# Kernel tuning notes

Hardware: AMD Instinct MI355X
Metric: run time of the kernel (lower is better)

## Reference

```python
import jax, jax.numpy as jnp
import numpy as np

B, S, D = 4, 8192, 512


def log_g(x):
    # torch: where(x>=0, log(relu(x)+0.5), -softplus(-x)); relu(x)+0.5 >= 0.5 so log is safe
    return jnp.where(x >= 0, jnp.log(jax.nn.relu(x) + 0.5), -jax.nn.softplus(-x))


def parallel_scan_log(log_coeffs, log_values):
    # log_coeffs: (B,S,D); log_values: (B,S+1,D)
    a_star = jnp.pad(jnp.cumsum(log_coeffs, axis=1), ((0, 0), (1, 0), (0, 0)))  # (B,S+1,D)
    log_h = a_star + jax.lax.cumlogsumexp(log_values - a_star, axis=1)
    return jnp.exp(log_h)[:, 1:]  # (B,S,D)


def setup_inputs() -> dict:
    key = jax.random.key(0)
    ks = jax.random.split(key, 7)
    scale = 1.0 / np.sqrt(D)
    x = jax.random.normal(ks[0], (B, S, D), dtype=jnp.float32)
    pre_h = jnp.zeros((B, 1, D), dtype=jnp.float32)
    Wf = jax.random.normal(ks[1], (D, D), dtype=jnp.float32) * scale
    bf = jax.random.normal(ks[2], (D,), dtype=jnp.float32) * 0.01
    Wi = jax.random.normal(ks[3], (D, D), dtype=jnp.float32) * scale
    bi = jax.random.normal(ks[4], (D,), dtype=jnp.float32) * 0.01
    Wh = jax.random.normal(ks[5], (D, D), dtype=jnp.float32) * scale
    bh = jax.random.normal(ks[6], (D,), dtype=jnp.float32) * 0.01
    return {"x": x, "pre_h": pre_h, "Wf": Wf, "bf": bf, "Wi": Wi, "bi": bi, "Wh": Wh, "bh": bh}


def reference(x, pre_h, Wf, bf, Wi, bi, Wh, bh):
    # gates: log(sigmoid(k)) = -softplus(-k)
    log_f = -jax.nn.softplus(-(jnp.einsum('bsd,de->bse', x, Wf) + bf))
    log_i = -jax.nn.softplus(-(jnp.einsum('bsd,de->bse', x, Wi) + bi))
    log_tilde_h = log_g(jnp.einsum('bsd,de->bse', x, Wh) + bh)
    log_pre_h = log_g(pre_h)  # (B,1,D)
    log_values = jnp.concatenate([log_pre_h, log_i + log_tilde_h], axis=1)  # (B,S+1,D)
    return parallel_scan_log(log_f, log_values)
```

## Files before the change

kernel.cpp:

```cpp
#include <hip/hip_runtime.h>
#include <hip/hip_bf16.h>

#define BATCH 4
#define SEQ   8192
#define DIM   512
#define M_TOT (BATCH*SEQ)
#define NCHUNK 128
#define CLEN   64

typedef __attribute__((ext_vector_type(4))) int int4v;
typedef __attribute__((ext_vector_type(8))) unsigned short ushort8v;

__device__ __forceinline__ float sigmoidf_(float x) {
    return 1.0f / (1.0f + __expf(-x));
}
__device__ __forceinline__ float gfun_(float x) {
    return (x >= 0.0f) ? (x + 0.5f) : sigmoidf_(x);
}

__device__ __forceinline__ void stage16(const void* g, void* lds) {
    __builtin_amdgcn_global_load_lds((const __attribute__((address_space(1))) void*)g,
                                     (__attribute__((address_space(3))) void*)lds,
                                     16, 0, 0);
}

__global__ __launch_bounds__(256) void quant_x(const float* __restrict__ x,
                                               char* __restrict__ xh, char* __restrict__ xl)
{
    const int t = blockIdx.x * 256 + threadIdx.x;
    float4 v = ((const float4*)x)[t];
    float vals[4] = {v.x, v.y, v.z, v.w};
    char hs[4], ls[4];
    #pragma unroll
    for (int e = 0; e < 4; ++e) {
        float c = fminf(fmaxf(vals[e], -15.8f), 15.8f);
        int q = (int)rintf(c * 2048.0f);
        int hi = (q + 128) >> 8;
        int lo = q - (hi << 8);
        hs[e] = (char)hi; ls[e] = (char)lo;
    }
    char4 hv = {hs[0], hs[1], hs[2], hs[3]};
    char4 lv = {ls[0], ls[1], ls[2], ls[3]};
    *(char4*)&xh[(size_t)t * 4] = hv;
    *(char4*)&xl[(size_t)t * 4] = lv;
}

__global__ __launch_bounds__(256) void quant_wT(
    const float* __restrict__ Wf, const float* __restrict__ Wi, const float* __restrict__ Wh,
    char* __restrict__ wth, char* __restrict__ wtl)
{
    __shared__ float tile[64][65];
    const int g = blockIdx.z;
    const float* W = (g == 0) ? Wf : (g == 1) ? Wi : Wh;
    const int k0 = blockIdx.x * 64, n0 = blockIdx.y * 64;
    const int c = threadIdx.x & 63, r4 = threadIdx.x >> 6;
    #pragma unroll
    for (int p = 0; p < 16; ++p) {
        int r = p * 4 + r4;
        tile[r][c] = W[(size_t)(k0 + r) * DIM + n0 + c];
    }
    __syncthreads();
    const size_t gbase = (size_t)g * DIM * DIM;
    #pragma unroll
    for (int p = 0; p < 16; ++p) {
        int nr = p * 4 + r4;
        float w = tile[c][nr];
        float cl = fminf(fmaxf(w, -0.49f), 0.49f);
        int q = (int)rintf(cl * 65536.0f);
        int hi = (q + 128) >> 8;
        int lo = q - (hi << 8);
        size_t o = gbase + (size_t)(n0 + nr) * DIM + k0 + c;
        wth[o] = (char)hi;
        wtl[o] = (char)lo;
    }
}

__global__ __launch_bounds__(512, 4) void gemm_i8(
    const char* __restrict__ xh, const char* __restrict__ xl,
    const char* __restrict__ wth, const char* __restrict__ wtl,
    const float* __restrict__ bfv, const float* __restrict__ biv, const float* __restrict__ bhv,
    float* __restrict__ fb, unsigned short* __restrict__ sib, unsigned short* __restrict__ ghb)
{
    __shared__ char smem[65536];
    char (*sA)[2][128][64] = (char (*)[2][128][64])smem;
    char (*sB)[2][128][64] = (char (*)[2][128][64])(smem + 32768);
    unsigned short (*lds16)[136] = (unsigned short (*)[136])smem;

    const int bid = blockIdx.x;
    const int xr  = bid & 7;
    const int t   = bid >> 3;
    const int mmt = t / 12;
    const int gn  = t - mmt * 12;
    const int g   = gn >> 2;
    const int n0  = (gn & 3) * 128;
    const int m0  = (xr + (mmt << 3)) * 128;

    const int tid  = threadIdx.x;
    const int wave = tid >> 6;
    const int lane = tid & 63;
    const int wi = wave >> 2, wj = wave & 3;

    const char* wh_g = wth + (size_t)g * DIM * DIM;
    const char* wl_g = wtl + (size_t)g * DIM * DIM;

    const int smm  = tid >> 2;
    const int skb  = (tid & 3) * 16;
    const int sksw = skb ^ (((smm >> 1) & 3) << 4);
    const int swrow = (tid >> 6) * 16;
    const char* gx_h = xh   + (size_t)(m0 + smm) * DIM + sksw;
    const char* gx_l = xl   + (size_t)(m0 + smm) * DIM + sksw;
    const char* gw_h = wh_g + (size_t)(n0 + smm) * DIM + sksw;
    const char* gw_l = wl_g + (size_t)(n0 + smm) * DIM + sksw;

    int4v P2[4][2], P1[4][2];
    const int4v zero = {0, 0, 0, 0};
    #pragma unroll
    for (int i = 0; i < 4; ++i)
        #pragma unroll
        for (int j = 0; j < 2; ++j) { P2[i][j] = zero; P1[i][j] = zero; }

    stage16(gx_h, &sA[0][0][swrow][0]);
    stage16(gx_l, &sA[0][1][swrow][0]);
    stage16(gw_h, &sB[0][0][swrow][0]);
    stage16(gw_l, &sB[0][1][swrow][0]);

    #pragma unroll
    for (int kt = 0; kt < 8; ++kt) {
        const int cur = kt & 1;
        if (kt < 7) {
            const int nb = cur ^ 1;
            const int ko = (kt + 1) * 64;
            stage16(gx_h + ko, &sA[nb][0][swrow][0]);
            stage16(gx_l + ko, &sA[nb][1][swrow][0]);
            stage16(gw_h + ko, &sB[nb][0][swrow][0]);
            stage16(gw_l + ko, &sB[nb][1][swrow][0]);
            asm volatile("s_waitcnt vmcnt(4)" ::: "memory");
        } else {
            asm volatile("s_waitcnt vmcnt(0)" ::: "memory");
        }
        asm volatile("s_barrier" ::: "memory");

        const int kseg = (lane >> 4) * 16;
        int4v bhf[2], blf[2];
        #pragma unroll
        for (int j = 0; j < 2; ++j) {
            const int col = wj * 32 + j * 16 + (lane & 15);
            const int ks  = kseg ^ (((col >> 1) & 3) << 4);
            bhf[j] = *(const int4v*)&sB[cur][0][col][ks];
            blf[j] = *(const int4v*)&sB[cur][1][col][ks];
        }
        __builtin_amdgcn_s_setprio(1);
        #pragma unroll
        for (int i = 0; i < 4; ++i) {
            const int row = wi * 64 + i * 16 + (lane & 15);
            const int ks  = kseg ^ (((row >> 1) & 3) << 4);
            int4v ahf = *(const int4v*)&sA[cur][0][row][ks];
            int4v alf = *(const int4v*)&sA[cur][1][row][ks];
            #pragma unroll
            for (int j = 0; j < 2; ++j) {
                P2[i][j] = __builtin_amdgcn_mfma_i32_16x16x64_i8(ahf, bhf[j], P2[i][j], 0, 0, 0);
                P1[i][j] = __builtin_amdgcn_mfma_i32_16x16x64_i8(ahf, blf[j], P1[i][j], 0, 0, 0);
                P1[i][j] = __builtin_amdgcn_mfma_i32_16x16x64_i8(alf, bhf[j], P1[i][j], 0, 0, 0);
            }
        }
        __builtin_amdgcn_s_setprio(0);
        asm volatile("s_barrier" ::: "memory");
    }

    const float c2 = 1.0f / 2048.0f;
    const float c1 = 1.0f / 524288.0f;
    const float* bias = (g == 0) ? bfv : (g == 1) ? biv : bhv;

    if (g == 0) {
        #pragma unroll
        for (int j = 0; j < 2; ++j) {
            const int col = n0 + wj * 32 + j * 16 + (lane & 15);
            const float bv = bias[col];
            #pragma unroll
            for (int i = 0; i < 4; ++i) {
                #pragma unroll
                for (int r = 0; r < 4; ++r) {
                    const float kv = (float)P2[i][j][r] * c2 + (float)P1[i][j][r] * c1 + bv;
                    const int row = m0 + wi * 64 + i * 16 + (lane >> 4) * 4 + r;
                    fb[(size_t)row * DIM + col] = sigmoidf_(kv);
                }
            }
        }
    } else {
        #pragma unroll
        for (int j = 0; j < 2; ++j) {
            const int lc = wj * 32 + j * 16 + (lane & 15);
            const float bv = bias[n0 + lc];
            #pragma unroll
            for (int i = 0; i < 4; ++i) {
                #pragma unroll
                for (int r = 0; r < 4; ++r) {
                    const float kv = (float)P2[i][j][r] * c2 + (float)P1[i][j][r] * c1 + bv;
                    const int lr = wi * 64 + i * 16 + (lane >> 4) * 4 + r;
                    unsigned short q;
                    if (g == 1) q = (unsigned short)fminf(rintf(sigmoidf_(kv) * 65536.0f), 65535.0f);
                    else        q = (unsigned short)fminf(rintf(gfun_(kv) * 8192.0f), 65535.0f);
                    lds16[lr][lc] = q;
                }
            }
        }
        __syncthreads();
        unsigned short* outp = (g == 1) ? sib : ghb;
        const int r  = tid >> 2;
        const int cq = tid & 3;
        #pragma unroll
        for (int it = 0; it < 4; ++it) {
            const int ci = cq + it * 4;
            ushort8v vv = *(const ushort8v*)&lds16[r][ci * 8];
            *(ushort8v*)&outp[(size_t)(m0 + r) * DIM + n0 + ci * 8] = vv;
        }
    }
}

#define VSCALE (1.0f / 536870912.0f)

__global__ __launch_bounds__(256) void scan_pass1(
    const float* __restrict__ fb,
    const unsigned short* __restrict__ sib, const unsigned short* __restrict__ ghb,
    float* __restrict__ Ach, float* __restrict__ Bch)
{
    const int dq  = threadIdx.x & 127;
    const int sub = threadIdx.x >> 7;
    const int c = blockIdx.x * 2 + sub;
    const int b = blockIdx.y;
    const int d = dq * 4;
    float A[4] = {1.f, 1.f, 1.f, 1.f};
    float B[4] = {0.f, 0.f, 0.f, 0.f};
    size_t base = ((size_t)(b * SEQ + c * CLEN)) * DIM + d;
    #pragma unroll 4
    for (int t = 0; t < CLEN; ++t) {
        float4  f4 = *(const float4*)&fb[base + (size_t)t * DIM];
        ushort4 s4 = *(const ushort4*)&sib[base + (size_t)t * DIM];
        ushort4 g4 = *(const ushort4*)&ghb[base + (size_t)t * DIM];
        float f[4] = {f4.x, f4.y, f4.z, f4.w};
        float v[4] = {(float)s4.x * (float)g4.x * VSCALE,
                      (float)s4.y * (float)g4.y * VSCALE,
                      (float)s4.z * (float)g4.z * VSCALE,
                      (float)s4.w * (float)g4.w * VSCALE};
        #pragma unroll
        for (int e = 0; e < 4; ++e) { B[e] = fmaf(f[e], B[e], v[e]); A[e] *= f[e]; }
    }
    const size_t idx = (size_t)(b * NCHUNK + c) * DIM + d;
    *(float4*)&Ach[idx] = *(float4*)A;
    *(float4*)&Bch[idx] = *(float4*)B;
}

__global__ __launch_bounds__(64) void scan_pass2(
    const float* __restrict__ pre_h,
    const float* __restrict__ Ach, const float* __restrict__ Bch,
    float* __restrict__ carry)
{
    const int gidx = blockIdx.x * 64 + threadIdx.x;
    const int b = gidx >> 9;
    const int d = gidx & (DIM - 1);
    float h = gfun_(pre_h[b * DIM + d]);
    #pragma unroll 4
    for (int c = 0; c < NCHUNK; ++c) {
        const int idx = (b * NCHUNK + c) * DIM + d;
        carry[idx] = h;
        h = fmaf(Ach[idx], h, Bch[idx]);
    }
}

__global__ __launch_bounds__(256) void scan_pass3(
    const float* __restrict__ fb,
    const unsigned short* __restrict__ sib, const unsigned short* __restrict__ ghb,
    const float* __restrict__ carry, float* __restrict__ out)
{
    const int dq  = threadIdx.x & 127;
    const int sub = threadIdx.x >> 7;
    const int c = blockIdx.x * 2 + sub;
    const int b = blockIdx.y;
    const int d = dq * 4;
    float4 h4 = *(const float4*)&carry[(size_t)(b * NCHUNK + c) * DIM + d];
    float h[4] = {h4.x, h4.y, h4.z, h4.w};
    size_t base = ((size_t)(b * SEQ + c * CLEN)) * DIM + d;
    #pragma unroll 4
    for (int t = 0; t < CLEN; ++t) {
        float4  f4 = *(const float4*)&fb[base + (size_t)t * DIM];
        ushort4 s4 = *(const ushort4*)&sib[base + (size_t)t * DIM];
        ushort4 g4 = *(const ushort4*)&ghb[base + (size_t)t * DIM];
        float f[4] = {f4.x, f4.y, f4.z, f4.w};
        float v[4] = {(float)s4.x * (float)g4.x * VSCALE,
                      (float)s4.y * (float)g4.y * VSCALE,
                      (float)s4.z * (float)g4.z * VSCALE,
                      (float)s4.w * (float)g4.w * VSCALE};
        float o[4];
        #pragma unroll
        for (int e = 0; e < 4; ++e) { h[e] = fmaf(f[e], h[e], v[e]); o[e] = h[e]; }
        *(float4*)&out[base + (size_t)t * DIM] = *(float4*)o;
    }
}

extern "C" void kernel_launch(void* const* d_in, const int* in_sizes, int n_in,
                              void* d_out, int out_size, void* d_ws, size_t ws_size,
                              hipStream_t stream) {
    const float* x     = (const float*)d_in[0];
    const float* pre_h = (const float*)d_in[1];
    const float* Wf    = (const float*)d_in[2];
    const float* bf    = (const float*)d_in[3];
    const float* Wi    = (const float*)d_in[4];
    const float* bi    = (const float*)d_in[5];
    const float* Wh    = (const float*)d_in[6];
    const float* bh    = (const float*)d_in[7];
    float* out = (float*)d_out;

    char* ws = (char*)d_ws;
    const size_t XQ = (size_t)M_TOT * DIM;
    const size_t WQ = (size_t)3 * DIM * DIM;
    const size_t FB = (size_t)M_TOT * DIM * sizeof(float);
    const size_t UB = (size_t)M_TOT * DIM * 2;
    const size_t CH = (size_t)BATCH * NCHUNK * DIM * sizeof(float);

    char*  xh  = ws;
    char*  xl  = ws + XQ;
    char*  wth = ws + 2 * XQ;
    char*  wtl = ws + 2 * XQ + WQ;
    float* fbuf = (float*)(ws + 2 * XQ + 2 * WQ);
    unsigned short* sibuf = (unsigned short*)((char*)fbuf + FB);
    unsigned short* ghbuf = (unsigned short*)((char*)sibuf + UB);
    float* Ach   = (float*)((char*)ghbuf + UB);
    float* Bch   = (float*)((char*)Ach + CH);
    float* carry = (float*)((char*)Bch + CH);

    quant_x<<<(M_TOT * DIM / 4) / 256, 256, 0, stream>>>(x, xh, xl);
    quant_wT<<<dim3(8, 8, 3), 256, 0, stream>>>(Wf, Wi, Wh, wth, wtl);
    gemm_i8<<<3072, 512, 0, stream>>>(xh, xl, wth, wtl, bf, bi, bh, fbuf, sibuf, ghbuf);
    scan_pass1<<<dim3(NCHUNK / 2, BATCH), 256, 0, stream>>>(fbuf, sibuf, ghbuf, Ach, Bch);
    scan_pass2<<<32, 64, 0, stream>>>(pre_h, Ach, Bch, carry);
    scan_pass3<<<dim3(NCHUNK / 2, BATCH), 256, 0, stream>>>(fbuf, sibuf, ghbuf, carry, out);
}
```

Measured before the change: 295.0 us.

## Quantize forget gate to 16-bit and halve scan chunk length

The forget-gate sigmoid output is now stored as a 16-bit fixed-point value, produced through the same LDS-staged coalesced write path as the other two gates, instead of as fp32 scattered stores. Both scan passes read it as ushort and rescale. This halves the intermediate's size and its write and read traffic. Separately, the scan chunk count is doubled (chunk length 32) to expose more parallelism in passes 1 and 3, at the cost of a longer serial carry pass 2. The quantization of f near 1 reduces precision, and errors compound over the long cumulative product.

Result: slower. 313.1 us (+6.1%).

```diff
diff --git a/kernel.cpp b/kernel.cpp
--- a/kernel.cpp
+++ b/kernel.cpp
@@ -5,8 +5,8 @@
 #define SEQ   8192
 #define DIM   512
 #define M_TOT (BATCH*SEQ)
-#define NCHUNK 128
-#define CLEN   64
+#define NCHUNK 256
+#define CLEN   32
 
 typedef __attribute__((ext_vector_type(4))) int int4v;
 typedef __attribute__((ext_vector_type(8))) unsigned short ushort8v;
@@ -79,7 +79,7 @@
     const char* __restrict__ xh, const char* __restrict__ xl,
     const char* __restrict__ wth, const char* __restrict__ wtl,
     const float* __restrict__ bfv, const float* __restrict__ biv, const float* __restrict__ bhv,
-    float* __restrict__ fb, unsigned short* __restrict__ sib, unsigned short* __restrict__ ghb)
+    unsigned short* __restrict__ fb, unsigned short* __restrict__ sib, unsigned short* __restrict__ ghb)
 {
     __shared__ char smem[65536];
     char (*sA)[2][128][64] = (char (*)[2][128][64])smem;
@@ -171,56 +171,40 @@
     const float c1 = 1.0f / 524288.0f;
     const float* bias = (g == 0) ? bfv : (g == 1) ? biv : bhv;
 
-    if (g == 0) {
-        #pragma unroll
-        for (int j = 0; j < 2; ++j) {
-            const int col = n0 + wj * 32 + j * 16 + (lane & 15);
-            const float bv = bias[col];
+    #pragma unroll
+    for (int j = 0; j < 2; ++j) {
+        const int lc = wj * 32 + j * 16 + (lane & 15);
+        const float bv = bias[n0 + lc];
+        #pragma unroll
+        for (int i = 0; i < 4; ++i) {
             #pragma unroll
-            for (int i = 0; i < 4; ++i) {
-                #pragma unroll
-                for (int r = 0; r < 4; ++r) {
-                    const float kv = (float)P2[i][j][r] * c2 + (float)P1[i][j][r] * c1 + bv;
-                    const int row = m0 + wi * 64 + i * 16 + (lane >> 4) * 4 + r;
-                    fb[(size_t)row * DIM + col] = sigmoidf_(kv);
-                }
+            for (int r = 0; r < 4; ++r) {
+                const float kv = (float)P2[i][j][r] * c2 + (float)P1[i][j][r] * c1 + bv;
+                const int lr = wi * 64 + i * 16 + (lane >> 4) * 4 + r;
+                unsigned short q;
+                if (g == 2) q = (unsigned short)fminf(rintf(gfun_(kv) * 8192.0f), 65535.0f);
+                else        q = (unsigned short)fminf(rintf(sigmoidf_(kv) * 65536.0f), 65535.0f);
+                lds16[lr][lc] = q;
             }
         }
-    } else {
-        #pragma unroll
-        for (int j = 0; j < 2; ++j) {
-            const int lc = wj * 32 + j * 16 + (lane & 15);
-            const float bv = bias[n0 + lc];
-            #pragma unroll
-            for (int i = 0; i < 4; ++i) {
-                #pragma unroll
-                for (int r = 0; r < 4; ++r) {
-                    const float kv = (float)P2[i][j][r] * c2 + (float)P1[i][j][r] * c1 + bv;
-                    const int lr = wi * 64 + i * 16 + (lane >> 4) * 4 + r;
-                    unsigned short q;
-                    if (g == 1) q = (unsigned short)fminf(rintf(sigmoidf_(kv) * 65536.0f), 65535.0f);
-                    else        q = (unsigned short)fminf(rintf(gfun_(kv) * 8192.0f), 65535.0f);
-                    lds16[lr][lc] = q;
-                }
-            }
-        }
-        __syncthreads();
-        unsigned short* outp = (g == 1) ? sib : ghb;
-        const int r  = tid >> 2;
-        const int cq = tid & 3;
-        #pragma unroll
-        for (int it = 0; it < 4; ++it) {
-            const int ci = cq + it * 4;
-            ushort8v vv = *(const ushort8v*)&lds16[r][ci * 8];
-            *(ushort8v*)&outp[(size_t)(m0 + r) * DIM + n0 + ci * 8] = vv;
-        }
-    }
-}
-
+    }
+    __syncthreads();
+    unsigned short* outp = (g == 0) ? fb : (g == 1) ? sib : ghb;
+    const int r  = tid >> 2;
+    const int cq = tid & 3;
+    #pragma unroll
+    for (int it = 0; it < 4; ++it) {
+        const int ci = cq + it * 4;
+        ushort8v vv = *(const ushort8v*)&lds16[r][ci * 8];
+        *(ushort8v*)&outp[(size_t)(m0 + r) * DIM + n0 + ci * 8] = vv;
+    }
+}
+
+#define FSCALE (1.0f / 65536.0f)
 #define VSCALE (1.0f / 536870912.0f)
 
 __global__ __launch_bounds__(256) void scan_pass1(
-    const float* __restrict__ fb,
+    const unsigned short* __restrict__ fb,
     const unsigned short* __restrict__ sib, const unsigned short* __restrict__ ghb,
     float* __restrict__ Ach, float* __restrict__ Bch)
 {
@@ -234,10 +218,11 @@
     size_t base = ((size_t)(b * SEQ + c * CLEN)) * DIM + d;
     #pragma unroll 4
     for (int t = 0; t < CLEN; ++t) {
-        float4  f4 = *(const float4*)&fb[base + (size_t)t * DIM];
+        ushort4 f4 = *(const ushort4*)&fb[base + (size_t)t * DIM];
         ushort4 s4 = *(const ushort4*)&sib[base + (size_t)t * DIM];
         ushort4 g4 = *(const ushort4*)&ghb[base + (size_t)t * DIM];
-        float f[4] = {f4.x, f4.y, f4.z, f4.w};
+        float f[4] = {(float)f4.x * FSCALE, (float)f4.y * FSCALE,
+                      (float)f4.z * FSCALE, (float)f4.w * FSCALE};
         float v[4] = {(float)s4.x * (float)g4.x * VSCALE,
                       (float)s4.y * (float)g4.y * VSCALE,
                       (float)s4.z * (float)g4.z * VSCALE,
@@ -268,7 +253,7 @@
 }
 
 __global__ __launch_bounds__(256) void scan_pass3(
-    const float* __restrict__ fb,
+    const unsigned short* __restrict__ fb,
     const unsigned short* __restrict__ sib, const unsigned short* __restrict__ ghb,
     const float* __restrict__ carry, float* __restrict__ out)
 {
@@ -282,10 +267,11 @@
     size_t base = ((size_t)(b * SEQ + c * CLEN)) * DIM + d;
     #pragma unroll 4
     for (int t = 0; t < CLEN; ++t) {
-        float4  f4 = *(const float4*)&fb[base + (size_t)t * DIM];
+        ushort4 f4 = *(const ushort4*)&fb[base + (size_t)t * DIM];
         ushort4 s4 = *(const ushort4*)&sib[base + (size_t)t * DIM];
         ushort4 g4 = *(const ushort4*)&ghb[base + (size_t)t * DIM];
-        float f[4] = {f4.x, f4.y, f4.z, f4.w};
+        float f[4] = {(float)f4.x * FSCALE, (float)f4.y * FSCALE,
+                      (float)f4.z * FSCALE, (float)f4.w * FSCALE};
         float v[4] = {(float)s4.x * (float)g4.x * VSCALE,
                       (float)s4.y * (float)g4.y * VSCALE,
                       (float)s4.z * (float)g4.z * VSCALE,
@@ -313,7 +299,6 @@
     char* ws = (char*)d_ws;
     const size_t XQ = (size_t)M_TOT * DIM;
     const size_t WQ = (size_t)3 * DIM * DIM;
-    const size_t FB = (size_t)M_TOT * DIM * sizeof(float);
     const size_t UB = (size_t)M_TOT * DIM * 2;
     const size_t CH = (size_t)BATCH * NCHUNK * DIM * sizeof(float);
 
@@ -321,8 +306,8 @@
     char*  xl  = ws + XQ;
     char*  wth = ws + 2 * XQ;
     char*  wtl = ws + 2 * XQ + WQ;
-    float* fbuf = (float*)(ws + 2 * XQ + 2 * WQ);
-    unsigned short* sibuf = (unsigned short*)((char*)fbuf + FB);
+    unsigned short* fbuf  = (unsigned short*)(ws + 2 * XQ + 2 * WQ);
+    unsigned short* sibuf = (unsigned short*)((char*)fbuf + UB);
     unsigned short* ghbuf = (unsigned short*)((char*)sibuf + UB);
     float* Ach   = (float*)((char*)ghbuf + UB);
     float* Bch   = (float*)((char*)Ach + CH);
```

## Fuse input and candidate gate GEMMs and store their product as one buffer

Applied to the files above, without the earlier changes.

The single gemm over three gates is split in two. The forget-gate GEMM runs alone. A new kernel computes the input-gate and candidate GEMMs together, sharing the staged x tiles, and writes the product sigmoid(ki)*g(kh) as a single 16-bit buffer. This removes one 16-bit intermediate write and read per element, cuts the scan kernels' traffic, and halves the x re-reads for those two gates. In exchange it uses 96KB of dynamic LDS and more accumulator registers (occupancy 2), adds a launch, and quantizes the fused value with a fixed 1/8192 scale, which could lose precision or clip large values.

Result: slower. 302.9 us (+2.7%).

```diff
diff --git a/kernel.cpp b/kernel.cpp
--- a/kernel.cpp
+++ b/kernel.cpp
@@ -4,6 +4,7 @@
 #define BATCH 4
 #define SEQ   8192
 #define DIM   512
+#define DD    (DIM*DIM)
 #define M_TOT (BATCH*SEQ)
 #define NCHUNK 128
 #define CLEN   64
@@ -60,7 +61,7 @@
         tile[r][c] = W[(size_t)(k0 + r) * DIM + n0 + c];
     }
     __syncthreads();
-    const size_t gbase = (size_t)g * DIM * DIM;
+    const size_t gbase = (size_t)g * DD;
     #pragma unroll
     for (int p = 0; p < 16; ++p) {
         int nr = p * 4 + r4;
@@ -75,24 +76,20 @@
     }
 }
 
-__global__ __launch_bounds__(512, 4) void gemm_i8(
+__global__ __launch_bounds__(512, 4) void gemm_f(
     const char* __restrict__ xh, const char* __restrict__ xl,
     const char* __restrict__ wth, const char* __restrict__ wtl,
-    const float* __restrict__ bfv, const float* __restrict__ biv, const float* __restrict__ bhv,
-    float* __restrict__ fb, unsigned short* __restrict__ sib, unsigned short* __restrict__ ghb)
+    const float* __restrict__ bfv, float* __restrict__ fb)
 {
     __shared__ char smem[65536];
     char (*sA)[2][128][64] = (char (*)[2][128][64])smem;
     char (*sB)[2][128][64] = (char (*)[2][128][64])(smem + 32768);
-    unsigned short (*lds16)[136] = (unsigned short (*)[136])smem;
 
     const int bid = blockIdx.x;
     const int xr  = bid & 7;
     const int t   = bid >> 3;
-    const int mmt = t / 12;
-    const int gn  = t - mmt * 12;
-    const int g   = gn >> 2;
-    const int n0  = (gn & 3) * 128;
+    const int mmt = t >> 2;
+    const int n0  = (t & 3) * 128;
     const int m0  = (xr + (mmt << 3)) * 128;
 
     const int tid  = threadIdx.x;
@@ -100,17 +97,14 @@
     const int lane = tid & 63;
     const int wi = wave >> 2, wj = wave & 3;
 
-    const char* wh_g = wth + (size_t)g * DIM * DIM;
-    const char* wl_g = wtl + (size_t)g * DIM * DIM;
-
     const int smm  = tid >> 2;
     const int skb  = (tid & 3) * 16;
     const int sksw = skb ^ (((smm >> 1) & 3) << 4);
     const int swrow = (tid >> 6) * 16;
-    const char* gx_h = xh   + (size_t)(m0 + smm) * DIM + sksw;
-    const char* gx_l = xl   + (size_t)(m0 + smm) * DIM + sksw;
-    const char* gw_h = wh_g + (size_t)(n0 + smm) * DIM + sksw;
-    const char* gw_l = wl_g + (size_t)(n0 + smm) * DIM + sksw;
+    const char* gx_h = xh  + (size_t)(m0 + smm) * DIM + sksw;
+    const char* gx_l = xl  + (size_t)(m0 + smm) * DIM + sksw;
+    const char* gw_h = wth + (size_t)(n0 + smm) * DIM + sksw;
+    const char* gw_l = wtl + (size_t)(n0 + smm) * DIM + sksw;
 
     int4v P2[4][2], P1[4][2];
     const int4v zero = {0, 0, 0, 0};
@@ -169,59 +163,157 @@
 
     const float c2 = 1.0f / 2048.0f;
     const float c1 = 1.0f / 524288.0f;
-    const float* bias = (g == 0) ? bfv : (g == 1) ? biv : bhv;
-
-    if (g == 0) {
+    #pragma unroll
+    for (int j = 0; j < 2; ++j) {
+        const int col = n0 + wj * 32 + j * 16 + (lane & 15);
+        const float bv = bfv[col];
+        #pragma unroll
+        for (int i = 0; i < 4; ++i) {
+            #pragma unroll
+            for (int r = 0; r < 4; ++r) {
+                const float kv = (float)P2[i][j][r] * c2 + (float)P1[i][j][r] * c1 + bv;
+                const int row = m0 + wi * 64 + i * 16 + (lane >> 4) * 4 + r;
+                fb[(size_t)row * DIM + col] = sigmoidf_(kv);
+            }
+        }
+    }
+}
+
+__global__ __launch_bounds__(512, 2) void gemm_ih(
+    const char* __restrict__ xh, const char* __restrict__ xl,
+    const char* __restrict__ wth, const char* __restrict__ wtl,
+    const float* __restrict__ biv, const float* __restrict__ bhv,
+    unsigned short* __restrict__ vb)
+{
+    extern __shared__ char smem[];
+    char (*sA)[2][128][64]    = (char (*)[2][128][64])smem;
+    char (*sB)[2][2][128][64] = (char (*)[2][2][128][64])(smem + 32768);
+    unsigned short (*lds16)[136] = (unsigned short (*)[136])smem;
+
+    const int bid = blockIdx.x;
+    const int xr  = bid & 7;
+    const int t   = bid >> 3;
+    const int mmt = t >> 2;
+    const int n0  = (t & 3) * 128;
+    const int m0  = (xr + (mmt << 3)) * 128;
+
+    const int tid  = threadIdx.x;
+    const int wave = tid >> 6;
+    const int lane = tid & 63;
+    const int wi = wave >> 2, wj = wave & 3;
+
+    const int smm  = tid >> 2;
+    const int skb  = (tid & 3) * 16;
+    const int sksw = skb ^ (((smm >> 1) & 3) << 4);
+    const int swrow = (tid >> 6) * 16;
+    const char* gx_h  = xh  + (size_t)(m0 + smm) * DIM + sksw;
+    const char* gx_l  = xl  + (size_t)(m0 + smm) * DIM + sksw;
+    const char* gwi_h = wth + (size_t)1 * DD + (size_t)(n0 + smm) * DIM + sksw;
+    const char* gwi_l = wtl + (size_t)1 * DD + (size_t)(n0 + smm) * DIM + sksw;
+    const char* gwh_h = wth + (size_t)2 * DD + (size_t)(n0 + smm) * DIM + sksw;
+    const char* gwh_l = wtl + (size_t)2 * DD + (size_t)(n0 + smm) * DIM + sksw;
+
+    int4v Pi2[4][2], Pi1[4][2], Ph2[4][2], Ph1[4][2];
+    const int4v zero = {0, 0, 0, 0};
+    #pragma unroll
+    for (int i = 0; i < 4; ++i)
         #pragma unroll
         for (int j = 0; j < 2; ++j) {
-            const int col = n0 + wj * 32 + j * 16 + (lane & 15);
-            const float bv = bias[col];
+            Pi2[i][j] = zero; Pi1[i][j] = zero;
+            Ph2[i][j] = zero; Ph1[i][j] = zero;
+        }
+
+    stage16(gx_h,  &sA[0][0][swrow][0]);
+    stage16(gx_l,  &sA[0][1][swrow][0]);
+    stage16(gwi_h, &sB[0][0][0][swrow][0]);
+    stage16(gwi_l, &sB[0][0][1][swrow][0]);
+    stage16(gwh_h, &sB[0][1][0][swrow][0]);
+    stage16(gwh_l, &sB[0][1][1][swrow][0]);
+
+    #pragma unroll
+    for (int kt = 0; kt < 8; ++kt) {
+        const int cur = kt & 1;
+        if (kt < 7) {
+            const int nb = cur ^ 1;
+            const int ko = (kt + 1) * 64;
+            stage16(gx_h  + ko, &sA[nb][0][swrow][0]);
+            stage16(gx_l  + ko, &sA[nb][1][swrow][0]);
+            stage16(gwi_h + ko, &sB[nb][0][0][swrow][0]);
+            stage16(gwi_l + ko, &sB[nb][0][1][swrow][0]);
+            stage16(gwh_h + ko, &sB[nb][1][0][swrow][0]);
+            stage16(gwh_l + ko, &sB[nb][1][1][swrow][0]);
+            asm volatile("s_waitcnt vmcnt(6)" ::: "memory");
+        } else {
+            asm volatile("s_waitcnt vmcnt(0)" ::: "memory");
+        }
+        asm volatile("s_barrier" ::: "memory");
+
+        const int kseg = (lane >> 4) * 16;
+        int4v bih[2], bil[2], bhh[2], bhl[2];
+        #pragma unroll
+        for (int j = 0; j < 2; ++j) {
+            const int col = wj * 32 + j * 16 + (lane & 15);
+            const int ks  = kseg ^ (((col >> 1) & 3) << 4);
+            bih[j] = *(const int4v*)&sB[cur][0][0][col][ks];
+            bil[j] = *(const int4v*)&sB[cur][0][1][col][ks];
+            bhh[j] = *(const int4v*)&sB[cur][1][0][col][ks];
+            bhl[j] = *(const int4v*)&sB[cur][1][1][col][ks];
+        }
+        __builtin_amdgcn_s_setprio(1);
+        #pragma unroll
+        for (int i = 0; i < 4; ++i) {
+            const int row = wi * 64 + i * 16 + (lane & 15);
+            const int ks  = kseg ^ (((row >> 1) & 3) << 4);
+            int4v ahf = *(const int4v*)&sA[cur][0][row][ks];
+            int4v alf = *(const int4v*)&sA[cur][1][row][ks];
             #pragma unroll
-            for (int i = 0; i < 4; ++i) {
-                #pragma unroll
-                for (int r = 0; r < 4; ++r) {
-                    const float kv = (float)P2[i][j][r] * c2 + (float)P1[i][j][r] * c1 + bv;
-                    const int row = m0 + wi * 64 + i * 16 + (lane >> 4) * 4 + r;
-                    fb[(size_t)row * DIM + col] = sigmoidf_(kv);
-                }
+            for (int j = 0; j < 2; ++j) {
+                Pi2[i][j] = __builtin_amdgcn_mfma_i32_16x16x64_i8(ahf, bih[j], Pi2[i][j], 0, 0, 0);
+                Pi1[i][j] = __builtin_amdgcn_mfma_i32_16x16x64_i8(ahf, bil[j], Pi1[i][j], 0, 0, 0);
+                Pi1[i][j] = __builtin_amdgcn_mfma_i32_16x16x64_i8(alf, bih[j], Pi1[i][j], 0, 0, 0);
+                Ph2[i][j] = __builtin_amdgcn_mfma_i32_16x16x64_i8(ahf, bhh[j], Ph2[i][j], 0, 0, 0);
+                Ph1[i][j] = __builtin_amdgcn_mfma_i32_16x16x64_i8(ahf, bhl[j], Ph1[i][j], 0, 0, 0);
+                Ph1[i][j] = __builtin_amdgcn_mfma_i32_16x16x64_i8(alf, bhh[j], Ph1[i][j], 0, 0, 0);
             }
         }
-    } else {
-        #pragma unroll
-        for (int j = 0; j < 2; ++j) {
-            const int lc = wj * 32 + j * 16 + (lane & 15);
-            const float bv = bias[n0 + lc];
+        __builtin_amdgcn_s_setprio(0);
+        asm volatile("s_barrier" ::: "memory");
+    }
+
+    const float c2 = 1.0f / 2048.0f;
+    const float c1 = 1.0f / 524288.0f;
+    #pragma unroll
+    for (int j = 0; j < 2; ++j) {
+        const int lc = wj * 32 + j * 16 + (lane & 15);
+        const float bvi = biv[n0 + lc];
+        const float bvh = bhv[n0 + lc];
+        #pragma unroll
+        for (int i = 0; i < 4; ++i) {
             #pragma unroll
-            for (int i = 0; i < 4; ++i) {
-                #pragma unroll
-                for (int r = 0; r < 4; ++r) {
-                    const float kv = (float)P2[i][j][r] * c2 + (float)P1[i][j][r] * c1 + bv;
-                    const int lr = wi * 64 + i * 16 + (lane >> 4) * 4 + r;
-                    unsigned short q;
-                    if (g == 1) q = (unsigned short)fminf(rintf(sigmoidf_(kv) * 65536.0f), 65535.0f);
-                    else        q = (unsigned short)fminf(rintf(gfun_(kv) * 8192.0f), 65535.0f);
-                    lds16[lr][lc] = q;
-                }
+            for (int r = 0; r < 4; ++r) {
+                const float ki = (float)Pi2[i][j][r] * c2 + (float)Pi1[i][j][r] * c1 + bvi;
+                const float kh = (float)Ph2[i][j][r] * c2 + (float)Ph1[i][j][r] * c1 + bvh;
+                const float v  = sigmoidf_(ki) * gfun_(kh);
+                const int lr = wi * 64 + i * 16 + (lane >> 4) * 4 + r;
+                lds16[lr][lc] = (unsigned short)fminf(rintf(v * 8192.0f), 65535.0f);
             }
         }
-        __syncthreads();
-        unsigned short* outp = (g == 1) ? sib : ghb;
-        const int r  = tid >> 2;
-        const int cq = tid & 3;
-        #pragma unroll
-        for (int it = 0; it < 4; ++it) {
-            const int ci = cq + it * 4;
-            ushort8v vv = *(const ushort8v*)&lds16[r][ci * 8];
-            *(ushort8v*)&outp[(size_t)(m0 + r) * DIM + n0 + ci * 8] = vv;
-        }
-    }
-}
-
-#define VSCALE (1.0f / 536870912.0f)
+    }
+    __syncthreads();
+    const int r  = tid >> 2;
+    const int cq = tid & 3;
+    #pragma unroll
+    for (int it = 0; it < 4; ++it) {
+        const int ci = cq + it * 4;
+        ushort8v vv = *(const ushort8v*)&lds16[r][ci * 8];
+        *(ushort8v*)&vb[(size_t)(m0 + r) * DIM + n0 + ci * 8] = vv;
+    }
+}
+
+#define VSCALE (1.0f / 8192.0f)
 
 __global__ __launch_bounds__(256) void scan_pass1(
-    const float* __restrict__ fb,
-    const unsigned short* __restrict__ sib, const unsigned short* __restrict__ ghb,
+    const float* __restrict__ fb, const unsigned short* __restrict__ vb,
     float* __restrict__ Ach, float* __restrict__ Bch)
 {
     const int dq  = threadIdx.x & 127;
@@ -235,13 +327,10 @@
     #pragma unroll 4
     for (int t = 0; t < CLEN; ++t) {
         float4  f4 = *(const float4*)&fb[base + (size_t)t * DIM];
-        ushort4 s4 = *(const ushort4*)&sib[base + (size_t)t * DIM];
-        ushort4 g4 = *(const ushort4*)&ghb[base + (size_t)t * DIM];
+        ushort4 v4 = *(const ushort4*)&vb[base + (size_t)t * DIM];
         float f[4] = {f4.x, f4.y, f4.z, f4.w};
-        float v[4] = {(float)s4.x * (float)g4.x * VSCALE,
-                      (float)s4.y * (float)g4.y * VSCALE,
-                      (float)s4.z * (float)g4.z * VSCALE,
-                      (float)s4.w * (float)g4.w * VSCALE};
+        float v[4] = {(float)v4.x * VSCALE, (float)v4.y * VSCALE,
+                      (float)v4.z * VSCALE, (float)v4.w * VSCALE};
         #pragma unroll
         for (int e = 0; e < 4; ++e) { B[e] = fmaf(f[e], B[e], v[e]); A[e] *= f[e]; }
     }
@@ -268,8 +357,7 @@
 }
 
 __global__ __launch_bounds__(256) void scan_pass3(
-    const float* __restrict__ fb,
-    const unsigned short* __restrict__ sib, const unsigned short* __restrict__ ghb,
+    const float* __restrict__ fb, const unsigned short* __restrict__ vb,
     const float* __restrict__ carry, float* __restrict__ out)
 {
     const int dq  = threadIdx.x & 127;
@@ -283,13 +371,10 @@
     #pragma unroll 4
     for (int t = 0; t < CLEN; ++t) {
         float4  f4 = *(const float4*)&fb[base + (size_t)t * DIM];
-        ushort4 s4 = *(const ushort4*)&sib[base + (size_t)t * DIM];
-        ushort4 g4 = *(const ushort4*)&ghb[base + (size_t)t * DIM];
+        ushort4 v4 = *(const ushort4*)&vb[base + (size_t)t * DIM];
         float f[4] = {f4.x, f4.y, f4.z, f4.w};
-        float v[4] = {(float)s4.x * (float)g4.x * VSCALE,
-                      (float)s4.y * (float)g4.y * VSCALE,
-                      (float)s4.z * (float)g4.z * VSCALE,
-                      (float)s4.w * (float)g4.w * VSCALE};
+        float v[4] = {(float)v4.x * VSCALE, (float)v4.y * VSCALE,
+                      (float)v4.z * VSCALE, (float)v4.w * VSCALE};
         float o[4];
         #pragma unroll
         for (int e = 0; e < 4; ++e) { h[e] = fmaf(f[e], h[e], v[e]); o[e] = h[e]; }
@@ -312,9 +397,9 @@
 
     char* ws = (char*)d_ws;
     const size_t XQ = (size_t)M_TOT * DIM;
-    const size_t WQ = (size_t)3 * DIM * DIM;
+    const size_t WQ = (size_t)3 * DD;
     const size_t FB = (size_t)M_TOT * DIM * sizeof(float);
-    const size_t UB = (size_t)M_TOT * DIM * 2;
+    const size_t VB = (size_t)M_TOT * DIM * 2;
     const size_t CH = (size_t)BATCH * NCHUNK * DIM * sizeof(float);
 
     char*  xh  = ws;
@@ -322,16 +407,23 @@
     char*  wth = ws + 2 * XQ;
     char*  wtl = ws + 2 * XQ + WQ;
     float* fbuf = (float*)(ws + 2 * XQ + 2 * WQ);
-    unsigned short* sibuf = (unsigned short*)((char*)fbuf + FB);
-    unsigned short* ghbuf = (unsigned short*)((char*)sibuf + UB);
-    float* Ach   = (float*)((char*)ghbuf + UB);
+    unsigned short* vbuf = (unsigned short*)((char*)fbuf + FB);
+    float* Ach   = (float*)((char*)vbuf + VB);
     float* Bch   = (float*)((char*)Ach + CH);
     float* carry = (float*)((char*)Bch + CH);
 
+    static bool attr_set = false;
+    if (!attr_set) {
+        hipFuncSetAttribute((const void*)gemm_ih,
+                            hipFuncAttributeMaxDynamicSharedMemorySize, 98304);
+        attr_set = true;
+    }
+
     quant_x<<<(M_TOT * DIM / 4) / 256, 256, 0, stream>>>(x, xh, xl);
     quant_wT<<<dim3(8, 8, 3), 256, 0, stream>>>(Wf, Wi, Wh, wth, wtl);
-    gemm_i8<<<3072, 512, 0, stream>>>(xh, xl, wth, wtl, bf, bi, bh, fbuf, sibuf, ghbuf);
-    scan_pass1<<<dim3(NCHUNK / 2, BATCH), 256, 0, stream>>>(fbuf, sibuf, ghbuf, Ach, Bch);
+    gemm_f<<<1024, 512, 0, stream>>>(xh, xl, wth, wtl, bf, fbuf);
+    gemm_ih<<<1024, 512, 98304, stream>>>(xh, xl, wth, wtl, bi, bh, vbuf);
+    scan_pass1<<<dim3(NCHUNK / 2, BATCH), 256, 0, stream>>>(fbuf, vbuf, Ach, Bch);
     scan_pass2<<<32, 64, 0, stream>>>(pre_h, Ach, Bch, carry);
-    scan_pass3<<<dim3(NCHUNK / 2, BATCH), 256, 0, stream>>>(fbuf, sibuf, ghbuf, carry, out);
-}
+    scan_pass3<<<dim3(NCHUNK / 2, BATCH), 256, 0, stream>>>(fbuf, vbuf, carry, out);
+}
```
